# Optimization experiments

Hardware: AMD Instinct MI355X
Metric: run time of the kernel (lower is better)

Reference implementation:

```python
import jax, jax.numpy as jnp
import numpy as np

NEG_SLOPE = 0.2

def gat_conv(x, src, dst, W, a_src, a_dst, b, num_nodes):
    # x: [N, in]; W: [in, H*F]; a_src/a_dst: [H, F]; b: [H*F]
    H, F = a_src.shape
    feat = (x @ W).reshape(-1, H, F)                 # [N, H, F]
    el = jnp.sum(feat * a_src, axis=-1)              # [N, H]
    er = jnp.sum(feat * a_dst, axis=-1)              # [N, H]
    e = jax.nn.leaky_relu(el[src] + er[dst], NEG_SLOPE)  # [E, H]
    # segment softmax over incoming edges of each dst node
    emax = jax.ops.segment_max(e, dst, num_segments=num_nodes)  # [N, H]
    ee = jnp.exp(e - emax[dst])
    denom = jax.ops.segment_sum(ee, dst, num_segments=num_nodes)  # [N, H]
    alpha = ee / denom[dst]                          # [E, H]
    msg = feat[src] * alpha[..., None]               # [E, H, F]
    out = jax.ops.segment_sum(msg, dst, num_segments=num_nodes)  # [N, H, F]
    return out + b.reshape(1, H, F)


def setup_inputs() -> dict:
    key = jax.random.key(0)
    ks = jax.random.split(key, 16)
    N, E = 50000, 800000
    IN, HID, OUT, H = 128, 32, 32, 4
    inp = {
        'features': jax.random.normal(ks[0], (N, IN), dtype=jnp.float32),
        'edge_src': jax.random.randint(ks[1], (E,), 0, N, dtype=jnp.int32),
        'edge_dst': jax.random.randint(ks[2], (E,), 0, N, dtype=jnp.int32),
        'W1': jax.random.normal(ks[3], (IN, H * HID), dtype=jnp.float32) * 0.1,
        'a1s': jax.random.normal(ks[4], (H, HID), dtype=jnp.float32) * 0.1,
        'a1d': jax.random.normal(ks[5], (H, HID), dtype=jnp.float32) * 0.1,
        'b1': jnp.zeros((H * HID,), dtype=jnp.float32),
        'W2': jax.random.normal(ks[6], (H * HID, H * HID), dtype=jnp.float32) * 0.1,
        'a2s': jax.random.normal(ks[7], (H, HID), dtype=jnp.float32) * 0.1,
        'a2d': jax.random.normal(ks[8], (H, HID), dtype=jnp.float32) * 0.1,
        'b2': jnp.zeros((H * HID,), dtype=jnp.float32),
        'W3': jax.random.normal(ks[9], (H * HID, OUT), dtype=jnp.float32) * 0.1,
        'a3s': jax.random.normal(ks[10], (1, OUT), dtype=jnp.float32) * 0.1,
        'a3d': jax.random.normal(ks[11], (1, OUT), dtype=jnp.float32) * 0.1,
        'b3': jnp.zeros((OUT,), dtype=jnp.float32),
    }
    return inp


def reference(features, edge_src, edge_dst, W1, a1s, a1d, b1, W2, a2s, a2d, b2, W3, a3s, a3d, b3):
    N = features.shape[0]
    # dropout=0.0 -> identity
    x = gat_conv(features, edge_src, edge_dst, W1, a1s, a1d, b1, N).reshape(N, -1)
    x = jax.nn.elu(x)
    x = gat_conv(x, edge_src, edge_dst, W2, a2s, a2d, b2, N).reshape(N, -1)
    x = jax.nn.elu(x)
    x = gat_conv(x, edge_src, edge_dst, W3, a3s, a3d, b3, N).mean(axis=1)  # [N, out]
    return x
```

## Files before the change

kernel.cpp:

```cpp
#include <hip/hip_runtime.h>

#define NEG_SLOPE 0.2f

typedef unsigned int uint;
typedef unsigned short ushort;

__device__ __forceinline__ float bperm_f(int idx, float v) {
    return __int_as_float(__builtin_amdgcn_ds_bpermute(idx, __float_as_int(v)));
}

__device__ __forceinline__ uint pack_bf16x2(float a, float b) {
    uint ba = __float_as_uint(a);
    uint bb = __float_as_uint(b);
    uint ra = (ba + 0x7FFFu + ((ba >> 16) & 1u)) >> 16;
    uint rb = (bb + 0x7FFFu + ((bb >> 16) & 1u)) >> 16;
    return ra | (rb << 16);
}

__device__ __forceinline__ void unpack_bf16x2(uint u, float& lo, float& hi) {
    lo = __uint_as_float(u << 16);
    hi = __uint_as_float(u & 0xFFFF0000u);
}


__global__ void zero_ints(int* __restrict__ p, int n) {
    int i = blockIdx.x * 256 + threadIdx.x;
    if (i < n) p[i] = 0;
}

__global__ void hist_kernel(const int* __restrict__ dst, int* __restrict__ deg,
                            int* __restrict__ rank, int E) {
    int i = blockIdx.x * 256 + threadIdx.x;
    if (i < E) rank[i] = atomicAdd(&deg[dst[i]], 1);
}

#define SCAN_CH 2048

__global__ __launch_bounds__(256) void scan_blocksum(const int* __restrict__ deg,
                                                     int* __restrict__ bsum, int N) {
    int blk = blockIdx.x, t = threadIdx.x;
    int base = blk * SCAN_CH;
    int s = 0;
#pragma unroll
    for (int i = 0; i < SCAN_CH / 256; ++i) {
        int idx = base + t + i * 256;
        if (idx < N) s += deg[idx];
    }
#pragma unroll
    for (int off = 1; off < 64; off <<= 1) s += __shfl_xor(s, off);
    __shared__ int wt[4];
    if ((t & 63) == 0) wt[t >> 6] = s;
    __syncthreads();
    if (t == 0) bsum[blk] = wt[0] + wt[1] + wt[2] + wt[3];
}

__global__ void scan_bsum(const int* __restrict__ bsum, int* __restrict__ boff, int nb) {
    int t = threadIdx.x;
    int orig = (t < nb) ? bsum[t] : 0;
    int v = orig;
#pragma unroll
    for (int off = 1; off < 64; off <<= 1) {
        int u = __shfl_up(v, off);
        if (t >= off) v += u;
    }
    if (t < nb) boff[t] = v - orig;
}

__global__ __launch_bounds__(256) void scan_write(const int* __restrict__ deg,
                                                  const int* __restrict__ boff,
                                                  int* __restrict__ rowptr, int N) {
    int blk = blockIdx.x, t = threadIdx.x;
    int base = blk * SCAN_CH + t * 8;
    int v[8];
    int s = 0;
#pragma unroll
    for (int r = 0; r < 8; ++r) {
        int idx = base + r;
        v[r] = (idx < N) ? deg[idx] : 0;
        s += v[r];
    }
    int lane = t & 63, wid = t >> 6;
    int p = s;
#pragma unroll
    for (int off = 1; off < 64; off <<= 1) {
        int u = __shfl_up(p, off);
        if (lane >= off) p += u;
    }
    __shared__ int wtot[4];
    if (lane == 63) wtot[wid] = p;
    __syncthreads();
    int run = boff[blk];
    for (int w = 0; w < wid; ++w) run += wtot[w];
    run += p - s;
#pragma unroll
    for (int r = 0; r < 8; ++r) {
        int idx = base + r;
        if (idx < N) {
            rowptr[idx] = run;
            run += v[r];
            if (idx == N - 1) rowptr[N] = run;
        }
    }
}

__global__ void fill_kernel(const int* __restrict__ src, const int* __restrict__ dst,
                            const int* __restrict__ rowptr, const int* __restrict__ rank,
                            int* __restrict__ csrc, int E) {
    int i = blockIdx.x * 256 + threadIdx.x;
    if (i < E) {
        int d = dst[i];
        __builtin_nontemporal_store(src[i], csrc + rowptr[d] + rank[i]);
    }
}


template <int OUTF, bool BF16OUT>
__global__ __launch_bounds__(256) void gemm_kernel(const float* __restrict__ X,
                                                   const float* __restrict__ W,
                                                   float* __restrict__ Y,
                                                   ushort* __restrict__ Yb,
                                                   const float* __restrict__ as_,
                                                   const float* __restrict__ ad_,
                                                   float* __restrict__ el,
                                                   float* __restrict__ er, int N) {
    constexpr int K = 128;
    constexpr int MG = OUTF / 4;
    constexpr int NPB = (256 / MG) * 4;
    constexpr int H = OUTF / 32;
    __shared__ float ws[K * OUTF];
    __shared__ float xs[NPB * K];
    int t = threadIdx.x;
    int nbase = blockIdx.x * NPB;

    {
        const float4* Wg = (const float4*)W;
        float4* wl = (float4*)ws;
        constexpr int WIT = K * OUTF / 4 / 256;
#pragma unroll
        for (int i = 0; i < WIT; ++i) wl[t + i * 256] = Wg[t + i * 256];
    }
    {
        const float4* Xg = (const float4*)X;
        float4* xl = (float4*)xs;
        constexpr int XIT = NPB * K / 4 / 256;
#pragma unroll
        for (int i = 0; i < XIT; ++i) {
            int idx = t + i * 256;
            int n = idx >> 5, kq = idx & 31;
            int gn = nbase + n;
            gn = min(gn, N - 1);
            xl[idx] = Xg[(size_t)gn * 32 + kq];
        }
    }
    __syncthreads();

    int mg = t % MG, ngq = t / MG;
    int n0 = ngq * 4;
    float acc[4][4];
#pragma unroll
    for (int i = 0; i < 4; ++i)
#pragma unroll
        for (int j = 0; j < 4; ++j) acc[i][j] = 0.f;

    const float4* xsv = (const float4*)xs;
    const float4* wsv = (const float4*)ws;
    for (int k = 0; k < K; k += 4) {
        float4 xv[4], wv[4];
#pragma unroll
        for (int i = 0; i < 4; ++i) xv[i] = xsv[(n0 + i) * 32 + (k >> 2)];
#pragma unroll
        for (int kk = 0; kk < 4; ++kk) wv[kk] = wsv[(k + kk) * MG + mg];
#pragma unroll
        for (int i = 0; i < 4; ++i) {
#pragma unroll
            for (int kk = 0; kk < 4; ++kk) {
                float xf = ((const float*)&xv[i])[kk];
                acc[i][0] = fmaf(xf, wv[kk].x, acc[i][0]);
                acc[i][1] = fmaf(xf, wv[kk].y, acc[i][1]);
                acc[i][2] = fmaf(xf, wv[kk].z, acc[i][2]);
                acc[i][3] = fmaf(xf, wv[kk].w, acc[i][3]);
            }
        }
    }

    int h = mg >> 3;
    if (OUTF == 32) h = 0;
    float4 as4 = ((const float4*)as_)[mg];
    float4 ad4 = ((const float4*)ad_)[mg];

#pragma unroll
    for (int i = 0; i < 4; ++i) {
        int gn = nbase + n0 + i;
        float pel = acc[i][0] * as4.x + acc[i][1] * as4.y + acc[i][2] * as4.z +
                    acc[i][3] * as4.w;
        float per = acc[i][0] * ad4.x + acc[i][1] * ad4.y + acc[i][2] * ad4.z +
                    acc[i][3] * ad4.w;
#pragma unroll
        for (int off = 1; off < 8; off <<= 1) {
            pel += __shfl_xor(pel, off);
            per += __shfl_xor(per, off);
        }
        if (gn < N) {
            if (BF16OUT) {
                uint2 pv;
                pv.x = pack_bf16x2(acc[i][0], acc[i][1]);
                pv.y = pack_bf16x2(acc[i][2], acc[i][3]);
                ((uint2*)Yb)[(size_t)gn * MG + mg] = pv;
            } else {
                float4 r;
                r.x = acc[i][0]; r.y = acc[i][1]; r.z = acc[i][2]; r.w = acc[i][3];
                ((float4*)Y)[(size_t)gn * MG + mg] = r;
            }
            if ((mg & 7) == 0) {
                el[gn * H + h] = pel;
                er[gn * H + h] = per;
            }
        }
    }
}


template <bool DOELU>
__global__ __launch_bounds__(256) void agg4_kernel(const ushort* __restrict__ featb,
                                                   const float* __restrict__ el,
                                                   const float* __restrict__ er,
                                                   const int* __restrict__ rowptr,
                                                   const int* __restrict__ csrc,
                                                   const float* __restrict__ bias,
                                                   float* __restrict__ out, int N) {
    int lane = threadIdx.x & 63;
    int node = blockIdx.x * 4 + (threadIdx.x >> 6);
    if (node >= N) return;
    int row0 = __builtin_amdgcn_readfirstlane(rowptr[node]);
    int row1 = __builtin_amdgcn_readfirstlane(rowptr[node + 1]);

    int qe = lane >> 2;
    int qh = lane & 3;
    float ern = er[node * 4 + qh];

    int g = lane >> 4;
    int li = lane & 15;
    int h = li >> 2;
    int ib = (g << 4) + (h << 2);

    float dacc = 0.f;
    float acc[8];
#pragma unroll
    for (int r = 0; r < 8; ++r) acc[r] = 0.f;

    for (int base = row0; base < row1; base += 16) {
        int e = base + qe;
        int s = 0;
        float w = 0.f;
        if (e < row1) {
            s = csrc[e];
            float tt = el[s * 4 + qh] + ern;
            tt = tt > 0.f ? tt : NEG_SLOPE * tt;
            w = __expf(tt);
            dacc += w;
        }
        int sj0 = __builtin_amdgcn_ds_bpermute(ib, s);
        float w0 = bperm_f(ib, w);
        int sj1 = __builtin_amdgcn_ds_bpermute(ib + 64, s);
        float w1 = bperm_f(ib + 64, w);
        int sj2 = __builtin_amdgcn_ds_bpermute(ib + 128, s);
        float w2 = bperm_f(ib + 128, w);
        int sj3 = __builtin_amdgcn_ds_bpermute(ib + 192, s);
        float w3 = bperm_f(ib + 192, w);
        uint4 U0 = *(const uint4*)(featb + (size_t)sj0 * 128 + li * 8);
        uint4 U1 = *(const uint4*)(featb + (size_t)sj1 * 128 + li * 8);
        uint4 U2 = *(const uint4*)(featb + (size_t)sj2 * 128 + li * 8);
        uint4 U3 = *(const uint4*)(featb + (size_t)sj3 * 128 + li * 8);
        float f0, f1, f2, f3, f4, f5, f6, f7;
        unpack_bf16x2(U0.x, f0, f1); unpack_bf16x2(U0.y, f2, f3);
        unpack_bf16x2(U0.z, f4, f5); unpack_bf16x2(U0.w, f6, f7);
        acc[0] = fmaf(w0, f0, acc[0]); acc[1] = fmaf(w0, f1, acc[1]);
        acc[2] = fmaf(w0, f2, acc[2]); acc[3] = fmaf(w0, f3, acc[3]);
        acc[4] = fmaf(w0, f4, acc[4]); acc[5] = fmaf(w0, f5, acc[5]);
        acc[6] = fmaf(w0, f6, acc[6]); acc[7] = fmaf(w0, f7, acc[7]);
        unpack_bf16x2(U1.x, f0, f1); unpack_bf16x2(U1.y, f2, f3);
        unpack_bf16x2(U1.z, f4, f5); unpack_bf16x2(U1.w, f6, f7);
        acc[0] = fmaf(w1, f0, acc[0]); acc[1] = fmaf(w1, f1, acc[1]);
        acc[2] = fmaf(w1, f2, acc[2]); acc[3] = fmaf(w1, f3, acc[3]);
        acc[4] = fmaf(w1, f4, acc[4]); acc[5] = fmaf(w1, f5, acc[5]);
        acc[6] = fmaf(w1, f6, acc[6]); acc[7] = fmaf(w1, f7, acc[7]);
        unpack_bf16x2(U2.x, f0, f1); unpack_bf16x2(U2.y, f2, f3);
        unpack_bf16x2(U2.z, f4, f5); unpack_bf16x2(U2.w, f6, f7);
        acc[0] = fmaf(w2, f0, acc[0]); acc[1] = fmaf(w2, f1, acc[1]);
        acc[2] = fmaf(w2, f2, acc[2]); acc[3] = fmaf(w2, f3, acc[3]);
        acc[4] = fmaf(w2, f4, acc[4]); acc[5] = fmaf(w2, f5, acc[5]);
        acc[6] = fmaf(w2, f6, acc[6]); acc[7] = fmaf(w2, f7, acc[7]);
        unpack_bf16x2(U3.x, f0, f1); unpack_bf16x2(U3.y, f2, f3);
        unpack_bf16x2(U3.z, f4, f5); unpack_bf16x2(U3.w, f6, f7);
        acc[0] = fmaf(w3, f0, acc[0]); acc[1] = fmaf(w3, f1, acc[1]);
        acc[2] = fmaf(w3, f2, acc[2]); acc[3] = fmaf(w3, f3, acc[3]);
        acc[4] = fmaf(w3, f4, acc[4]); acc[5] = fmaf(w3, f5, acc[5]);
        acc[6] = fmaf(w3, f6, acc[6]); acc[7] = fmaf(w3, f7, acc[7]);
    }

#pragma unroll
    for (int r = 0; r < 8; ++r) {
        acc[r] += __shfl_xor(acc[r], 16);
        acc[r] += __shfl_xor(acc[r], 32);
    }
#pragma unroll
    for (int off = 4; off < 64; off <<= 1) dacc += __shfl_xor(dacc, off);
    float d = bperm_f((li >> 2) << 2, dacc);

    if (lane < 16) {
        float inv = (row1 > row0) ? 1.f / d : 0.f;
        const float4* bv = (const float4*)bias + li * 2;
        float4 b0 = bv[0], b1 = bv[1];
        float o[8];
#pragma unroll
        for (int r = 0; r < 8; ++r) o[r] = acc[r] * inv;
        o[0] += b0.x; o[1] += b0.y; o[2] += b0.z; o[3] += b0.w;
        o[4] += b1.x; o[5] += b1.y; o[6] += b1.z; o[7] += b1.w;
        if (DOELU) {
#pragma unroll
            for (int r = 0; r < 8; ++r) o[r] = o[r] > 0.f ? o[r] : __expf(o[r]) - 1.f;
        }
        float4 q0, q1;
        q0.x = o[0]; q0.y = o[1]; q0.z = o[2]; q0.w = o[3];
        q1.x = o[4]; q1.y = o[5]; q1.z = o[6]; q1.w = o[7];
        float4* ov = (float4*)(out + (size_t)node * 128) + li * 2;
        ov[0] = q0;
        ov[1] = q1;
    }
}


__global__ __launch_bounds__(256) void agg1_kernel(const float* __restrict__ feat,
                                                   const float* __restrict__ el,
                                                   const float* __restrict__ er,
                                                   const int* __restrict__ rowptr,
                                                   const int* __restrict__ csrc,
                                                   const float* __restrict__ bias,
                                                   float* __restrict__ out, int N) {
    int lane = threadIdx.x & 63;
    int node = blockIdx.x * 4 + (threadIdx.x >> 6);
    if (node >= N) return;
    int row0 = __builtin_amdgcn_readfirstlane(rowptr[node]);
    int row1 = __builtin_amdgcn_readfirstlane(rowptr[node + 1]);

    float ern = er[node];
    int g = lane >> 3;
    int li = lane & 7;

    float dacc = 0.f;
    float acc[4];
#pragma unroll
    for (int r = 0; r < 4; ++r) acc[r] = 0.f;

    for (int base = row0; base < row1; base += 64) {
        int e = base + lane;
        int s = 0;
        float w0 = 0.f;
        if (e < row1) {
            s = csrc[e];
            float t0 = el[s] + ern;
            t0 = t0 > 0.f ? t0 : NEG_SLOPE * t0;
            w0 = __expf(t0);
            dacc += w0;
        }
        int cnt = min(row1 - base, 64);
        int iters = (cnt + 7) >> 3;
        int it = 0;
        for (; it + 1 < iters; it += 2) {
            int idxA = ((it << 3) + g) << 2;
            int idxB = (((it + 1) << 3) + g) << 2;
            int sjA = __builtin_amdgcn_ds_bpermute(idxA, s);
            float wA = bperm_f(idxA, w0);
            int sjB = __builtin_amdgcn_ds_bpermute(idxB, s);
            float wB = bperm_f(idxB, w0);
            const float4* fpA = (const float4*)(feat + (size_t)sjA * 32) + li;
            const float4* fpB = (const float4*)(feat + (size_t)sjB * 32) + li;
            float4 a0 = fpA[0], b0 = fpB[0];
            acc[0] = fmaf(wA, a0.x, acc[0]); acc[1] = fmaf(wA, a0.y, acc[1]);
            acc[2] = fmaf(wA, a0.z, acc[2]); acc[3] = fmaf(wA, a0.w, acc[3]);
            acc[0] = fmaf(wB, b0.x, acc[0]); acc[1] = fmaf(wB, b0.y, acc[1]);
            acc[2] = fmaf(wB, b0.z, acc[2]); acc[3] = fmaf(wB, b0.w, acc[3]);
        }
        if (it < iters) {
            int idx = ((it << 3) + g) << 2;
            int sj = __builtin_amdgcn_ds_bpermute(idx, s);
            float wsel = bperm_f(idx, w0);
            const float4* fp = (const float4*)(feat + (size_t)sj * 32) + li;
            float4 v0 = fp[0];
            acc[0] = fmaf(wsel, v0.x, acc[0]); acc[1] = fmaf(wsel, v0.y, acc[1]);
            acc[2] = fmaf(wsel, v0.z, acc[2]); acc[3] = fmaf(wsel, v0.w, acc[3]);
        }
    }

#pragma unroll
    for (int r = 0; r < 4; ++r) {
        acc[r] += __shfl_xor(acc[r], 8);
        acc[r] += __shfl_xor(acc[r], 16);
        acc[r] += __shfl_xor(acc[r], 32);
    }
#pragma unroll
    for (int off = 1; off < 64; off <<= 1) dacc += __shfl_xor(dacc, off);

    if (lane < 8) {
        float inv = (row1 > row0) ? 1.f / dacc : 0.f;
        float4 b0 = ((const float4*)bias)[lane];
        float4 q;
        q.x = acc[0] * inv + b0.x;
        q.y = acc[1] * inv + b0.y;
        q.z = acc[2] * inv + b0.z;
        q.w = acc[3] * inv + b0.w;
        ((float4*)(out + (size_t)node * 32))[lane] = q;
    }
}


extern "C" void kernel_launch(void* const* d_in, const int* in_sizes, int n_in,
                              void* d_out, int out_size, void* d_ws, size_t ws_size,
                              hipStream_t stream) {
    const float* features = (const float*)d_in[0];
    const int* esrc = (const int*)d_in[1];
    const int* edst = (const int*)d_in[2];
    const float* W1 = (const float*)d_in[3];
    const float* a1s = (const float*)d_in[4];
    const float* a1d = (const float*)d_in[5];
    const float* b1 = (const float*)d_in[6];
    const float* W2 = (const float*)d_in[7];
    const float* a2s = (const float*)d_in[8];
    const float* a2d = (const float*)d_in[9];
    const float* b2 = (const float*)d_in[10];
    const float* W3 = (const float*)d_in[11];
    const float* a3s = (const float*)d_in[12];
    const float* a3d = (const float*)d_in[13];
    const float* b3 = (const float*)d_in[14];

    int N = in_sizes[0] / 128;
    int E = in_sizes[1];
    int nb = (N + SCAN_CH - 1) / SCAN_CH;

    char* base = (char*)d_ws;
    size_t off = 0;
    auto nxt = [&](size_t bytes) {
        void* p = base + off;
        off += (bytes + 255) & ~(size_t)255;
        return p;
    };
    ushort* Yb = (ushort*)nxt((size_t)N * 128 * 2);
    float* B = (float*)nxt((size_t)N * 128 * 4);
    float* A2 = (float*)nxt((size_t)N * 32 * 4);
    float* el = (float*)nxt((size_t)N * 4 * 4);
    float* er = (float*)nxt((size_t)N * 4 * 4);
    int* deg = (int*)nxt((size_t)N * 4);
    int* rowptr = (int*)nxt((size_t)(N + 1) * 4);
    int* csrc = (int*)nxt((size_t)E * 4);
    int* rank = (int*)nxt((size_t)E * 4);
    int* bsum = (int*)nxt((size_t)(nb + 1) * 4);
    int* boff = (int*)nxt((size_t)(nb + 1) * 4);

    zero_ints<<<(N + 255) / 256, 256, 0, stream>>>(deg, N);
    hist_kernel<<<(E + 255) / 256, 256, 0, stream>>>(edst, deg, rank, E);
    scan_blocksum<<<nb, 256, 0, stream>>>(deg, bsum, N);
    scan_bsum<<<1, 64, 0, stream>>>(bsum, boff, nb);
    scan_write<<<nb, 256, 0, stream>>>(deg, boff, rowptr, N);
    fill_kernel<<<(E + 255) / 256, 256, 0, stream>>>(esrc, edst, rowptr, rank, csrc, E);

    gemm_kernel<128, true><<<(N + 31) / 32, 256, 0, stream>>>(features, W1, nullptr, Yb,
                                                              a1s, a1d, el, er, N);
    agg4_kernel<true><<<(N + 3) / 4, 256, 0, stream>>>(Yb, el, er, rowptr, csrc, b1, B, N);

    gemm_kernel<128, true><<<(N + 31) / 32, 256, 0, stream>>>(B, W2, nullptr, Yb,
                                                              a2s, a2d, el, er, N);
    agg4_kernel<true><<<(N + 3) / 4, 256, 0, stream>>>(Yb, el, er, rowptr, csrc, b2, B, N);

    gemm_kernel<32, false><<<(N + 127) / 128, 256, 0, stream>>>(B, W3, A2, nullptr,
                                                                a3s, a3d, el, er, N);
    agg1_kernel<<<(N + 3) / 4, 256, 0, stream>>>(A2, el, er, rowptr, csrc, b3,
                                                 (float*)d_out, N);
}
```

Measured before the change: 253.0 us.

## Replace FP32 LDS GEMMs with bf16 MFMA and store intermediate activations in bf16

Swaps the three shared-memory FP32 SIMT GEMM kernels for a bf16 MFMA 16x16x32 kernel. Weights are prepacked into fragment layout by a small kernel, and the input features are converted to bf16 up front. The aggregation kernels now write bf16 activations for the next layer, and layer 3 features are stored as bf16, which cuts memory traffic for the GEMM inputs and the final-layer gathers. This costs precision in the GEMM inputs and the layer-3 features, and adds several small launches plus scattered 2-byte stores from the MFMA output layout.

New measurement: 229.3 us. -9.4%, faster.

```diff
diff --git a/kernel.cpp b/kernel.cpp
--- a/kernel.cpp
+++ b/kernel.cpp
@@ -4,6 +4,8 @@
 
 typedef unsigned int uint;
 typedef unsigned short ushort;
+typedef __attribute__((ext_vector_type(8))) short bf16x8;
+typedef __attribute__((ext_vector_type(4))) float f32x4;
 
 __device__ __forceinline__ float bperm_f(int idx, float v) {
     return __int_as_float(__builtin_amdgcn_ds_bpermute(idx, __float_as_int(v)));
@@ -15,6 +17,11 @@
     uint ra = (ba + 0x7FFFu + ((ba >> 16) & 1u)) >> 16;
     uint rb = (bb + 0x7FFFu + ((bb >> 16) & 1u)) >> 16;
     return ra | (rb << 16);
+}
+
+__device__ __forceinline__ ushort bf16_rne(float v) {
+    uint b = __float_as_uint(v);
+    return (ushort)((b + 0x7FFFu + ((b >> 16) & 1u)) >> 16);
 }
 
 __device__ __forceinline__ void unpack_bf16x2(uint u, float& lo, float& hi) {
@@ -114,109 +121,116 @@
 }
 
 
-template <int OUTF, bool BF16OUT>
-__global__ __launch_bounds__(256) void gemm_kernel(const float* __restrict__ X,
-                                                   const float* __restrict__ W,
-                                                   float* __restrict__ Y,
-                                                   ushort* __restrict__ Yb,
-                                                   const float* __restrict__ as_,
-                                                   const float* __restrict__ ad_,
-                                                   float* __restrict__ el,
-                                                   float* __restrict__ er, int N) {
-    constexpr int K = 128;
-    constexpr int MG = OUTF / 4;
-    constexpr int NPB = (256 / MG) * 4;
+__global__ __launch_bounds__(256) void cvt_bf16_kernel(const float* __restrict__ X,
+                                                       ushort* __restrict__ Xb, int n8) {
+    int i = blockIdx.x * 256 + threadIdx.x;
+    if (i >= n8) return;
+    const float4* xp = (const float4*)X + (size_t)i * 2;
+    float4 v0 = xp[0], v1 = xp[1];
+    uint4 q;
+    q.x = pack_bf16x2(v0.x, v0.y);
+    q.y = pack_bf16x2(v0.z, v0.w);
+    q.z = pack_bf16x2(v1.x, v1.y);
+    q.w = pack_bf16x2(v1.z, v1.w);
+    ((uint4*)Xb)[i] = q;
+}
+
+
+template <int OUTF>
+__global__ __launch_bounds__(256) void wpack_kernel(const float* __restrict__ W,
+                                                    ushort* __restrict__ wfrag) {
+    constexpr int TOT = (OUTF / 16) * 4 * 64;
+    int idx = blockIdx.x * 256 + threadIdx.x;
+    if (idx >= TOT) return;
+    int lane = idx & 63;
+    int kt = (idx >> 6) & 3;
+    int ct = idx >> 8;
+    int col = ct * 16 + (lane & 15);
+    int k0 = kt * 32 + (lane >> 4) * 8;
+    uint4 q;
+    q.x = pack_bf16x2(W[(k0 + 0) * OUTF + col], W[(k0 + 1) * OUTF + col]);
+    q.y = pack_bf16x2(W[(k0 + 2) * OUTF + col], W[(k0 + 3) * OUTF + col]);
+    q.z = pack_bf16x2(W[(k0 + 4) * OUTF + col], W[(k0 + 5) * OUTF + col]);
+    q.w = pack_bf16x2(W[(k0 + 6) * OUTF + col], W[(k0 + 7) * OUTF + col]);
+    ((uint4*)wfrag)[idx] = q;
+}
+
+
+template <int OUTF>
+__global__ __launch_bounds__(256) void gemm_mfma_kernel(const ushort* __restrict__ Xb,
+                                                        const ushort* __restrict__ wfrag,
+                                                        ushort* __restrict__ Yb,
+                                                        const float* __restrict__ as_,
+                                                        const float* __restrict__ ad_,
+                                                        float* __restrict__ el,
+                                                        float* __restrict__ er, int N) {
     constexpr int H = OUTF / 32;
-    __shared__ float ws[K * OUTF];
-    __shared__ float xs[NPB * K];
-    int t = threadIdx.x;
-    int nbase = blockIdx.x * NPB;
-
+    constexpr int NCT = OUTF / 16;
+    int lane = threadIdx.x & 63;
+    int wv = threadIdx.x >> 6;
+    int r0 = blockIdx.x * 64 + wv * 16;
+    if (r0 >= N) return;
+    int lrow = lane & 15;
+    int lk8 = lane >> 4;
+
+    bf16x8 afrag[4];
     {
-        const float4* Wg = (const float4*)W;
-        float4* wl = (float4*)ws;
-        constexpr int WIT = K * OUTF / 4 / 256;
-#pragma unroll
-        for (int i = 0; i < WIT; ++i) wl[t + i * 256] = Wg[t + i * 256];
-    }
-    {
-        const float4* Xg = (const float4*)X;
-        float4* xl = (float4*)xs;
-        constexpr int XIT = NPB * K / 4 / 256;
-#pragma unroll
-        for (int i = 0; i < XIT; ++i) {
-            int idx = t + i * 256;
-            int n = idx >> 5, kq = idx & 31;
-            int gn = nbase + n;
-            gn = min(gn, N - 1);
-            xl[idx] = Xg[(size_t)gn * 32 + kq];
-        }
-    }
-    __syncthreads();
-
-    int mg = t % MG, ngq = t / MG;
-    int n0 = ngq * 4;
-    float acc[4][4];
-#pragma unroll
-    for (int i = 0; i < 4; ++i)
-#pragma unroll
-        for (int j = 0; j < 4; ++j) acc[i][j] = 0.f;
-
-    const float4* xsv = (const float4*)xs;
-    const float4* wsv = (const float4*)ws;
-    for (int k = 0; k < K; k += 4) {
-        float4 xv[4], wv[4];
-#pragma unroll
-        for (int i = 0; i < 4; ++i) xv[i] = xsv[(n0 + i) * 32 + (k >> 2)];
-#pragma unroll
-        for (int kk = 0; kk < 4; ++kk) wv[kk] = wsv[(k + kk) * MG + mg];
-#pragma unroll
-        for (int i = 0; i < 4; ++i) {
-#pragma unroll
-            for (int kk = 0; kk < 4; ++kk) {
-                float xf = ((const float*)&xv[i])[kk];
-                acc[i][0] = fmaf(xf, wv[kk].x, acc[i][0]);
-                acc[i][1] = fmaf(xf, wv[kk].y, acc[i][1]);
-                acc[i][2] = fmaf(xf, wv[kk].z, acc[i][2]);
-                acc[i][3] = fmaf(xf, wv[kk].w, acc[i][3]);
+        int arow = min(r0 + lrow, N - 1);
+        const ushort* xr = Xb + (size_t)arow * 128;
+#pragma unroll
+        for (int kt = 0; kt < 4; ++kt)
+            afrag[kt] = *(const bf16x8*)(xr + kt * 32 + lk8 * 8);
+    }
+
+    float pel[H][4];
+    float prr[H][4];
+#pragma unroll
+    for (int h = 0; h < H; ++h)
+#pragma unroll
+        for (int j = 0; j < 4; ++j) { pel[h][j] = 0.f; prr[h][j] = 0.f; }
+
+    const bf16x8* wf = (const bf16x8*)wfrag;
+#pragma unroll
+    for (int ct = 0; ct < NCT; ++ct) {
+        f32x4 acc = {0.f, 0.f, 0.f, 0.f};
+#pragma unroll
+        for (int kt = 0; kt < 4; ++kt) {
+            bf16x8 b = wf[(ct * 4 + kt) * 64 + lane];
+            acc = __builtin_amdgcn_mfma_f32_16x16x32_bf16(afrag[kt], b, acc, 0, 0, 0);
+        }
+        int col = ct * 16 + lrow;
+        constexpr int hh = 0;
+        int h = (H == 1) ? 0 : (ct >> 1);
+        float asc = as_[col], adc = ad_[col];
+#pragma unroll
+        for (int j = 0; j < 4; ++j) {
+            int row = r0 + lk8 * 4 + j;
+            float v = acc[j];
+            if (row < N) Yb[(size_t)row * OUTF + col] = bf16_rne(v);
+            pel[h][j] = fmaf(v, asc, pel[h][j]);
+            prr[h][j] = fmaf(v, adc, prr[h][j]);
+        }
+        (void)hh;
+    }
+
+#pragma unroll
+    for (int h = 0; h < H; ++h)
+#pragma unroll
+        for (int j = 0; j < 4; ++j) {
+            float pe = pel[h][j], pr = prr[h][j];
+#pragma unroll
+            for (int off = 1; off < 16; off <<= 1) {
+                pe += __shfl_xor(pe, off);
+                pr += __shfl_xor(pr, off);
             }
-        }
-    }
-
-    int h = mg >> 3;
-    if (OUTF == 32) h = 0;
-    float4 as4 = ((const float4*)as_)[mg];
-    float4 ad4 = ((const float4*)ad_)[mg];
-
-#pragma unroll
-    for (int i = 0; i < 4; ++i) {
-        int gn = nbase + n0 + i;
-        float pel = acc[i][0] * as4.x + acc[i][1] * as4.y + acc[i][2] * as4.z +
-                    acc[i][3] * as4.w;
-        float per = acc[i][0] * ad4.x + acc[i][1] * ad4.y + acc[i][2] * ad4.z +
-                    acc[i][3] * ad4.w;
-#pragma unroll
-        for (int off = 1; off < 8; off <<= 1) {
-            pel += __shfl_xor(pel, off);
-            per += __shfl_xor(per, off);
-        }
-        if (gn < N) {
-            if (BF16OUT) {
-                uint2 pv;
-                pv.x = pack_bf16x2(acc[i][0], acc[i][1]);
-                pv.y = pack_bf16x2(acc[i][2], acc[i][3]);
-                ((uint2*)Yb)[(size_t)gn * MG + mg] = pv;
-            } else {
-                float4 r;
-                r.x = acc[i][0]; r.y = acc[i][1]; r.z = acc[i][2]; r.w = acc[i][3];
-                ((float4*)Y)[(size_t)gn * MG + mg] = r;
+            if (lrow == 0) {
+                int row = r0 + lk8 * 4 + j;
+                if (row < N) {
+                    el[row * H + h] = pe;
+                    er[row * H + h] = pr;
+                }
             }
-            if ((mg & 7) == 0) {
-                el[gn * H + h] = pel;
-                er[gn * H + h] = per;
-            }
-        }
-    }
+        }
 }
 
 
@@ -227,7 +241,7 @@
                                                    const int* __restrict__ rowptr,
                                                    const int* __restrict__ csrc,
                                                    const float* __restrict__ bias,
-                                                   float* __restrict__ out, int N) {
+                                                   ushort* __restrict__ outb, int N) {
     int lane = threadIdx.x & 63;
     int node = blockIdx.x * 4 + (threadIdx.x >> 6);
     if (node >= N) return;
@@ -320,17 +334,17 @@
 #pragma unroll
             for (int r = 0; r < 8; ++r) o[r] = o[r] > 0.f ? o[r] : __expf(o[r]) - 1.f;
         }
-        float4 q0, q1;
-        q0.x = o[0]; q0.y = o[1]; q0.z = o[2]; q0.w = o[3];
-        q1.x = o[4]; q1.y = o[5]; q1.z = o[6]; q1.w = o[7];
-        float4* ov = (float4*)(out + (size_t)node * 128) + li * 2;
-        ov[0] = q0;
-        ov[1] = q1;
-    }
-}
-
-
-__global__ __launch_bounds__(256) void agg1_kernel(const float* __restrict__ feat,
+        uint4 q;
+        q.x = pack_bf16x2(o[0], o[1]);
+        q.y = pack_bf16x2(o[2], o[3]);
+        q.z = pack_bf16x2(o[4], o[5]);
+        q.w = pack_bf16x2(o[6], o[7]);
+        *(uint4*)(outb + (size_t)node * 128 + li * 8) = q;
+    }
+}
+
+
+__global__ __launch_bounds__(256) void agg1_kernel(const ushort* __restrict__ featb,
                                                    const float* __restrict__ el,
                                                    const float* __restrict__ er,
                                                    const int* __restrict__ rowptr,
@@ -373,22 +387,25 @@
             float wA = bperm_f(idxA, w0);
             int sjB = __builtin_amdgcn_ds_bpermute(idxB, s);
             float wB = bperm_f(idxB, w0);
-            const float4* fpA = (const float4*)(feat + (size_t)sjA * 32) + li;
-            const float4* fpB = (const float4*)(feat + (size_t)sjB * 32) + li;
-            float4 a0 = fpA[0], b0 = fpB[0];
-            acc[0] = fmaf(wA, a0.x, acc[0]); acc[1] = fmaf(wA, a0.y, acc[1]);
-            acc[2] = fmaf(wA, a0.z, acc[2]); acc[3] = fmaf(wA, a0.w, acc[3]);
-            acc[0] = fmaf(wB, b0.x, acc[0]); acc[1] = fmaf(wB, b0.y, acc[1]);
-            acc[2] = fmaf(wB, b0.z, acc[2]); acc[3] = fmaf(wB, b0.w, acc[3]);
+            uint2 UA = *(const uint2*)(featb + (size_t)sjA * 32 + li * 4);
+            uint2 UB = *(const uint2*)(featb + (size_t)sjB * 32 + li * 4);
+            float f0, f1, f2, f3;
+            unpack_bf16x2(UA.x, f0, f1); unpack_bf16x2(UA.y, f2, f3);
+            acc[0] = fmaf(wA, f0, acc[0]); acc[1] = fmaf(wA, f1, acc[1]);
+            acc[2] = fmaf(wA, f2, acc[2]); acc[3] = fmaf(wA, f3, acc[3]);
+            unpack_bf16x2(UB.x, f0, f1); unpack_bf16x2(UB.y, f2, f3);
+            acc[0] = fmaf(wB, f0, acc[0]); acc[1] = fmaf(wB, f1, acc[1]);
+            acc[2] = fmaf(wB, f2, acc[2]); acc[3] = fmaf(wB, f3, acc[3]);
         }
         if (it < iters) {
             int idx = ((it << 3) + g) << 2;
             int sj = __builtin_amdgcn_ds_bpermute(idx, s);
             float wsel = bperm_f(idx, w0);
-            const float4* fp = (const float4*)(feat + (size_t)sj * 32) + li;
-            float4 v0 = fp[0];
-            acc[0] = fmaf(wsel, v0.x, acc[0]); acc[1] = fmaf(wsel, v0.y, acc[1]);
-            acc[2] = fmaf(wsel, v0.z, acc[2]); acc[3] = fmaf(wsel, v0.w, acc[3]);
+            uint2 U = *(const uint2*)(featb + (size_t)sj * 32 + li * 4);
+            float f0, f1, f2, f3;
+            unpack_bf16x2(U.x, f0, f1); unpack_bf16x2(U.y, f2, f3);
+            acc[0] = fmaf(wsel, f0, acc[0]); acc[1] = fmaf(wsel, f1, acc[1]);
+            acc[2] = fmaf(wsel, f2, acc[2]); acc[3] = fmaf(wsel, f3, acc[3]);
         }
     }
 
@@ -444,9 +461,10 @@
         off += (bytes + 255) & ~(size_t)255;
         return p;
     };
+    ushort* Xb = (ushort*)nxt((size_t)N * 128 * 2);
     ushort* Yb = (ushort*)nxt((size_t)N * 128 * 2);
-    float* B = (float*)nxt((size_t)N * 128 * 4);
-    float* A2 = (float*)nxt((size_t)N * 32 * 4);
+    ushort* Bb = (ushort*)nxt((size_t)N * 128 * 2);
+    ushort* Y3b = (ushort*)nxt((size_t)N * 32 * 2);
     float* el = (float*)nxt((size_t)N * 4 * 4);
     float* er = (float*)nxt((size_t)N * 4 * 4);
     int* deg = (int*)nxt((size_t)N * 4);
@@ -455,24 +473,30 @@
     int* rank = (int*)nxt((size_t)E * 4);
     int* bsum = (int*)nxt((size_t)(nb + 1) * 4);
     int* boff = (int*)nxt((size_t)(nb + 1) * 4);
+    ushort* wf1 = (ushort*)nxt(16384 * 2);
+    ushort* wf2 = (ushort*)nxt(16384 * 2);
+    ushort* wf3 = (ushort*)nxt(4096 * 2);
+
+    int gemm_grid = (N + 63) / 64;
 
     zero_ints<<<(N + 255) / 256, 256, 0, stream>>>(deg, N);
     hist_kernel<<<(E + 255) / 256, 256, 0, stream>>>(edst, deg, rank, E);
+    cvt_bf16_kernel<<<(N * 16 + 255) / 256, 256, 0, stream>>>(features, Xb, N * 16);
+    wpack_kernel<128><<<8, 256, 0, stream>>>(W1, wf1);
+    wpack_kernel<128><<<8, 256, 0, stream>>>(W2, wf2);
+    wpack_kernel<32><<<2, 256, 0, stream>>>(W3, wf3);
     scan_blocksum<<<nb, 256, 0, stream>>>(deg, bsum, N);
     scan_bsum<<<1, 64, 0, stream>>>(bsum, boff, nb);
     scan_write<<<nb, 256, 0, stream>>>(deg, boff, rowptr, N);
     fill_kernel<<<(E + 255) / 256, 256, 0, stream>>>(esrc, edst, rowptr, rank, csrc, E);
 
-    gemm_kernel<128, true><<<(N + 31) / 32, 256, 0, stream>>>(features, W1, nullptr, Yb,
-                                                              a1s, a1d, el, er, N);
-    agg4_kernel<true><<<(N + 3) / 4, 256, 0, stream>>>(Yb, el, er, rowptr, csrc, b1, B, N);
-
-    gemm_kernel<128, true><<<(N + 31) / 32, 256, 0, stream>>>(B, W2, nullptr, Yb,
-                                                              a2s, a2d, el, er, N);
-    agg4_kernel<true><<<(N + 3) / 4, 256, 0, stream>>>(Yb, el, er, rowptr, csrc, b2, B, N);
-
-    gemm_kernel<32, false><<<(N + 127) / 128, 256, 0, stream>>>(B, W3, A2, nullptr,
-                                                                a3s, a3d, el, er, N);
-    agg1_kernel<<<(N + 3) / 4, 256, 0, stream>>>(A2, el, er, rowptr, csrc, b3,
+    gemm_mfma_kernel<128><<<gemm_grid, 256, 0, stream>>>(Xb, wf1, Yb, a1s, a1d, el, er, N);
+    agg4_kernel<true><<<(N + 3) / 4, 256, 0, stream>>>(Yb, el, er, rowptr, csrc, b1, Bb, N);
+
+    gemm_mfma_kernel<128><<<gemm_grid, 256, 0, stream>>>(Bb, wf2, Yb, a2s, a2d, el, er, N);
+    agg4_kernel<true><<<(N + 3) / 4, 256, 0, stream>>>(Yb, el, er, rowptr, csrc, b2, Bb, N);
+
+    gemm_mfma_kernel<32><<<gemm_grid, 256, 0, stream>>>(Bb, wf3, Y3b, a3s, a3d, el, er, N);
+    agg1_kernel<<<(N + 3) / 4, 256, 0, stream>>>(Y3b, el, er, rowptr, csrc, b3,
                                                  (float*)d_out, N);
 }
```
